# Kernel optimization log

Hardware: AMD Instinct MI355X
Metric: run time of the kernel (lower is better)

## Reference

```python
import jax, jax.numpy as jnp
import numpy as np

NC, M, D = 4, 512, 64
COMMITMENT_COST = 0.25


def setup_inputs() -> dict:
    key = jax.random.key(0)
    k1, k2 = jax.random.split(key)
    N = 65536
    x = jax.random.normal(k1, (N, NC * D), dtype=jnp.float32)
    # original init: uniform(-1/m, 1/m); randn*small keeps comparable scale
    embedding = jax.random.normal(k2, (NC, M, D), dtype=jnp.float32) * (1.0 / M)
    mask = jnp.ones((N, NC), dtype=jnp.float32)
    return {"x": x, "embedding": embedding, "mask": mask}


def reference(x, embedding, mask):
    nc, m, d = embedding.shape
    x_flat = x.reshape(-1, nc, d)                      # (N, nc, d)
    xd = jax.lax.stop_gradient(x_flat)                 # detached copy

    # squared-distance search expressed as a GEMM (same math as sum((x-e)^2)):
    x2 = jnp.sum(xd * xd, axis=-1)[:, :, None]
    e2 = jnp.sum(embedding * embedding, axis=-1)[None, :, :]
    xe = jnp.einsum('ncd,cmd->ncm', xd, embedding)
    distances = x2 - 2.0 * xe + e2

    indices = jnp.argmin(distances, axis=-1)           # (N, nc) int
    # gather nearest code vectors: (N, nc, d)
    quantized = embedding[jnp.arange(nc)[None, :], indices]
    quantized = quantized * mask[..., None]

    codebook_loss = jnp.mean((jax.lax.stop_gradient(x_flat) - quantized) ** 2)
    e_latent_loss = jnp.mean((x_flat - jax.lax.stop_gradient(quantized)) ** 2)
    commitment_loss = COMMITMENT_COST * e_latent_loss

    # straight-through estimator
    quantized_st = x_flat + jax.lax.stop_gradient(quantized - x_flat)
    quantized_st = quantized_st.reshape(x.shape)

    # perplexity via per-codebook histogram (avoids N x nc x m one-hot)
    counts = jax.vmap(lambda idx: jnp.bincount(idx, length=m))(indices.T)  # (nc, m)
    avg_probs = counts.astype(x.dtype) / x_flat.shape[0]
    perplexity = jnp.exp(-jnp.sum(avg_probs * jnp.log(avg_probs + 1e-10)))

    return (quantized_st, commitment_loss, codebook_loss, perplexity, indices)
```

## Files before the change

kernel.cpp:

```cpp
#include <hip/hip_runtime.h>
#include <math.h>
#include <float.h>

#define NTOK 65536
#define NCB  4
#define MCODE 512
#define DIM  64

#define QST_SIZE (NTOK * NCB * DIM)
#define IDX_OFF  (QST_SIZE + 3)

#define TOK_TILE  128

#define WS_EH 0
#define WS_EL 262144
#define WS_D0 524288
#define WS_CNT 532480
#define WS_LOSS 540672

typedef _Float16 half8 __attribute__((ext_vector_type(8)));
typedef float floatx16 __attribute__((ext_vector_type(16)));

__global__ __launch_bounds__(256) void prep_kernel(const float* __restrict__ emb,
                                                   _Float16* __restrict__ ehf,
                                                   _Float16* __restrict__ elf,
                                                   float* __restrict__ d0p,
                                                   int* __restrict__ counts,
                                                   float* __restrict__ lossSum) {
    int row = blockIdx.x * 256 + threadIdx.x;
    if (row >= NCB * MCODE) return;
    const int c   = row >> 9;
    const int n   = row & 511;
    const int nt  = n >> 5;
    const int r5  = n & 31;
    const float* src = emb + (size_t)row * DIM;

    float s = 0.f;
#pragma unroll
    for (int ch = 0; ch < 4; ++ch) {
#pragma unroll
        for (int h = 0; h < 2; ++h) {
            half8 hv, lv;
#pragma unroll
            for (int t = 0; t < 8; ++t) {
                float e = src[ch * 16 + h * 8 + t];
                s += e * e;
                float f = e * 512.0f;
                _Float16 hi = (_Float16)f;
                float r = f - (float)hi;
                hv[t] = hi;
                lv[t] = (_Float16)r;
            }
            size_t off = ((size_t)((c * 16 + nt) * 4 + ch)) * 512 + (h * 32 + r5) * 8;
            *(half8*)(ehf + off) = hv;
            *(half8*)(elf + off) = lv;
        }
    }
    d0p[row] = -256.0f * s;
    counts[row] = 0;
    if (row == 0) *lossSum = 0.f;
}

__global__ __launch_bounds__(256) void vq_main(const float* __restrict__ x,
                                               const float* __restrict__ emb,
                                               const float* __restrict__ mask,
                                               const _Float16* __restrict__ ehf,
                                               const _Float16* __restrict__ elf,
                                               const float* __restrict__ d0p,
                                               int* __restrict__ counts,
                                               float* __restrict__ lossSum,
                                               float* __restrict__ outQ,
                                               float* __restrict__ outIdx) {
    __shared__ int   Is[TOK_TILE];
    __shared__ float wls[4];

    const int tid  = threadIdx.x;
    const int c    = blockIdx.y;
    const int n0tk = blockIdx.x * TOK_TILE;
    const int lane = tid & 63;
    const int w    = tid >> 6;
    const int l31  = lane & 31;
    const int hi   = lane >> 5;
    const int hi4  = hi * 4;

    half8 Bh[4], Bl[4];
    {
        const float* xr = x + (size_t)(n0tk + w * 32 + l31) * (NCB * DIM) + c * DIM + hi * 8;
#pragma unroll
        for (int ch = 0; ch < 4; ++ch) {
            float fv[8];
            *(float4*)(fv)     = *(const float4*)(xr + ch * 16);
            *(float4*)(fv + 4) = *(const float4*)(xr + ch * 16 + 4);
            half8 h8, l8;
#pragma unroll
            for (int t = 0; t < 8; ++t) {
                float f = fv[t];
                _Float16 hh = (_Float16)f;
                h8[t] = hh;
                l8[t] = (_Float16)(f - (float)hh);
            }
            Bh[ch] = h8;
            Bl[ch] = l8;
        }
    }

    const _Float16* Ah_base = ehf + (size_t)c * (16 * 4 * 512) + (size_t)lane * 8;
    const _Float16* Al_base = elf + (size_t)c * (16 * 4 * 512) + (size_t)lane * 8;
    const float*    d0c     = d0p + c * MCODE;

    float maxv = -FLT_MAX;
    int   maxn = 0;

    for (int nt = 0; nt < 16; ++nt) {
        const _Float16* pah = Ah_base + (size_t)nt * 2048;
        const _Float16* pal = Al_base + (size_t)nt * 2048;
        half8 Ah0 = *(const half8*)(pah);
        half8 Ah1 = *(const half8*)(pah + 512);
        half8 Ah2 = *(const half8*)(pah + 1024);
        half8 Ah3 = *(const half8*)(pah + 1536);
        half8 Al0 = *(const half8*)(pal);
        half8 Al1 = *(const half8*)(pal + 512);
        half8 Al2 = *(const half8*)(pal + 1024);
        half8 Al3 = *(const half8*)(pal + 1536);

        const float* dpt = d0c + nt * 32 + hi4;
        float4 d40 = *(const float4*)(dpt);
        float4 d41 = *(const float4*)(dpt + 8);
        float4 d42 = *(const float4*)(dpt + 16);
        float4 d43 = *(const float4*)(dpt + 24);
        floatx16 acc;
        acc[0]  = d40.x; acc[1]  = d40.y; acc[2]  = d40.z; acc[3]  = d40.w;
        acc[4]  = d41.x; acc[5]  = d41.y; acc[6]  = d41.z; acc[7]  = d41.w;
        acc[8]  = d42.x; acc[9]  = d42.y; acc[10] = d42.z; acc[11] = d42.w;
        acc[12] = d43.x; acc[13] = d43.y; acc[14] = d43.z; acc[15] = d43.w;

        acc = __builtin_amdgcn_mfma_f32_32x32x16_f16(Ah0, Bh[0], acc, 0, 0, 0);
        acc = __builtin_amdgcn_mfma_f32_32x32x16_f16(Al0, Bh[0], acc, 0, 0, 0);
        acc = __builtin_amdgcn_mfma_f32_32x32x16_f16(Ah0, Bl[0], acc, 0, 0, 0);
        acc = __builtin_amdgcn_mfma_f32_32x32x16_f16(Ah1, Bh[1], acc, 0, 0, 0);
        acc = __builtin_amdgcn_mfma_f32_32x32x16_f16(Al1, Bh[1], acc, 0, 0, 0);
        acc = __builtin_amdgcn_mfma_f32_32x32x16_f16(Ah1, Bl[1], acc, 0, 0, 0);
        acc = __builtin_amdgcn_mfma_f32_32x32x16_f16(Ah2, Bh[2], acc, 0, 0, 0);
        acc = __builtin_amdgcn_mfma_f32_32x32x16_f16(Al2, Bh[2], acc, 0, 0, 0);
        acc = __builtin_amdgcn_mfma_f32_32x32x16_f16(Ah2, Bl[2], acc, 0, 0, 0);
        acc = __builtin_amdgcn_mfma_f32_32x32x16_f16(Ah3, Bh[3], acc, 0, 0, 0);
        acc = __builtin_amdgcn_mfma_f32_32x32x16_f16(Al3, Bh[3], acc, 0, 0, 0);
        acc = __builtin_amdgcn_mfma_f32_32x32x16_f16(Ah3, Bl[3], acc, 0, 0, 0);

        const int nbase = nt * 32 + hi4;
#pragma unroll
        for (int r = 0; r < 16; ++r) {
            float m = acc[r];
            int   n = nbase + ((r & 3) + 8 * (r >> 2));
            if (m > maxv) { maxv = m; maxn = n; }
        }
    }

    {
        float ov = __shfl_xor(maxv, 32);
        int   on = __shfl_xor(maxn, 32);
        if (ov > maxv || (ov == maxv && on < maxn)) { maxv = ov; maxn = on; }
    }

    if (hi == 0) {
        Is[w * 32 + l31] = maxn;
        atomicAdd(&counts[c * MCODE + maxn], 1);
        outIdx[(size_t)(n0tk + w * 32 + l31) * NCB + c] = (float)maxn;
    }
    __syncthreads();

    float lloss = 0.f;
#pragma unroll
    for (int i = 0; i < 8; ++i) {
        int q = tid + i * 256;
        int tok = q >> 4, d4 = q & 15;
        int idx = Is[tok];
        float mv = mask[(size_t)(n0tk + tok) * NCB + c];
        float4 e4 = *(const float4*)(emb + ((size_t)c * MCODE + idx) * DIM + d4 * 4);
        float4 x4 = *(const float4*)(x + (size_t)(n0tk + tok) * (NCB * DIM) + c * DIM + d4 * 4);
        float qx = e4.x * mv, qy = e4.y * mv, qz = e4.z * mv, qw = e4.w * mv;
        float4 o;
        o.x = x4.x + (qx - x4.x);
        o.y = x4.y + (qy - x4.y);
        o.z = x4.z + (qz - x4.z);
        o.w = x4.w + (qw - x4.w);
        *(float4*)(outQ + (size_t)(n0tk + tok) * (NCB * DIM) + c * DIM + d4 * 4) = o;
        float dx = x4.x - qx, dy = x4.y - qy, dz = x4.z - qz, dw = x4.w - qw;
        lloss += dx * dx + dy * dy + dz * dz + dw * dw;
    }
#pragma unroll
    for (int off = 32; off > 0; off >>= 1) lloss += __shfl_xor(lloss, off);
    if ((tid & 63) == 0) wls[tid >> 6] = lloss;
    __syncthreads();
    if (tid == 0) {
        float s = wls[0] + wls[1] + wls[2] + wls[3];
        atomicAdd(lossSum, s);
    }
}

__global__ __launch_bounds__(256) void finalize_kernel(const int* __restrict__ counts,
                                                       const float* __restrict__ lossSum,
                                                       float* __restrict__ out) {
    __shared__ float wls[4];
    int tid = threadIdx.x;
    float s = 0.f;
#pragma unroll
    for (int i = 0; i < 8; ++i) {
        int j = tid + i * 256;
        float p = (float)counts[j] * (1.0f / 65536.0f);
        s += p * logf(p + 1e-10f);
    }
#pragma unroll
    for (int off = 32; off > 0; off >>= 1) s += __shfl_xor(s, off);
    if ((tid & 63) == 0) wls[tid >> 6] = s;
    __syncthreads();
    if (tid == 0) {
        float tot = wls[0] + wls[1] + wls[2] + wls[3];
        float L = *lossSum * (1.0f / (float)QST_SIZE);
        out[QST_SIZE + 0] = 0.25f * L;
        out[QST_SIZE + 1] = L;
        out[QST_SIZE + 2] = expf(-tot);
    }
}

extern "C" void kernel_launch(void* const* d_in, const int* in_sizes, int n_in,
                              void* d_out, int out_size, void* d_ws, size_t ws_size,
                              hipStream_t stream) {
    const float* x    = (const float*)d_in[0];
    const float* emb  = (const float*)d_in[1];
    const float* mask = (const float*)d_in[2];
    float* out = (float*)d_out;

    _Float16* ehf  = (_Float16*)((char*)d_ws + WS_EH);
    _Float16* elf  = (_Float16*)((char*)d_ws + WS_EL);
    float* d0p     = (float*)((char*)d_ws + WS_D0);
    int*   counts  = (int*)((char*)d_ws + WS_CNT);
    float* lossSum = (float*)((char*)d_ws + WS_LOSS);

    prep_kernel<<<dim3(8), dim3(256), 0, stream>>>(emb, ehf, elf, d0p, counts, lossSum);
    vq_main<<<dim3(NTOK / TOK_TILE, NCB), dim3(256), 0, stream>>>(
        x, emb, mask, ehf, elf, d0p, counts, lossSum, out, out + IDX_OFF);
    finalize_kernel<<<dim3(1), dim3(256), 0, stream>>>(counts, lossSum, out);
}
```

Baseline: 211.3 us.

## Stage codebook tiles through double-buffered LDS with prefetch

Each block now loads the per-codebook fp16 hi/lo embedding tiles and the distance bias cooperatively into shared memory. The next tile is prefetched from global memory while the current one runs through MFMA, replacing the per-wave direct global loads in which every wave read the same codebook data. This cuts redundant global/L2 traffic and hides load latency, at the cost of a block-wide barrier per iteration and extra LDS use that may lower occupancy.

Result: faster. 202.6 us (-4.1%).

```diff
diff --git a/kernel.cpp b/kernel.cpp
--- a/kernel.cpp
+++ b/kernel.cpp
@@ -71,6 +71,8 @@
                                                float* __restrict__ lossSum,
                                                float* __restrict__ outQ,
                                                float* __restrict__ outIdx) {
+    __shared__ __align__(16) _Float16 As[2][4096];
+    __shared__ __align__(16) float d0s[MCODE];
     __shared__ int   Is[TOK_TILE];
     __shared__ float wls[4];
 
@@ -83,6 +85,14 @@
     const int hi   = lane >> 5;
     const int hi4  = hi * 4;
 
+    const _Float16* gEh = ehf + (size_t)c * (16 * 4 * 512);
+    const _Float16* gEl = elf + (size_t)c * (16 * 4 * 512);
+
+    float4 sh = *(const float4*)(gEh + tid * 8);
+    float4 sl = *(const float4*)(gEl + tid * 8);
+    float4 dstage;
+    if (tid < 128) dstage = *(const float4*)(d0p + c * MCODE + tid * 4);
+
     half8 Bh[4], Bl[4];
     {
         const float* xr = x + (size_t)(n0tk + w * 32 + l31) * (NCB * DIM) + c * DIM + hi * 8;
@@ -104,26 +114,35 @@
         }
     }
 
-    const _Float16* Ah_base = ehf + (size_t)c * (16 * 4 * 512) + (size_t)lane * 8;
-    const _Float16* Al_base = elf + (size_t)c * (16 * 4 * 512) + (size_t)lane * 8;
-    const float*    d0c     = d0p + c * MCODE;
+    *(float4*)((char*)&As[0][0]    + tid * 16) = sh;
+    *(float4*)((char*)&As[0][2048] + tid * 16) = sl;
+    if (tid < 128) *(float4*)(&d0s[tid * 4]) = dstage;
+    __syncthreads();
 
     float maxv = -FLT_MAX;
     int   maxn = 0;
 
     for (int nt = 0; nt < 16; ++nt) {
-        const _Float16* pah = Ah_base + (size_t)nt * 2048;
-        const _Float16* pal = Al_base + (size_t)nt * 2048;
-        half8 Ah0 = *(const half8*)(pah);
-        half8 Ah1 = *(const half8*)(pah + 512);
-        half8 Ah2 = *(const half8*)(pah + 1024);
-        half8 Ah3 = *(const half8*)(pah + 1536);
-        half8 Al0 = *(const half8*)(pal);
-        half8 Al1 = *(const half8*)(pal + 512);
-        half8 Al2 = *(const half8*)(pal + 1024);
-        half8 Al3 = *(const half8*)(pal + 1536);
-
-        const float* dpt = d0c + nt * 32 + hi4;
+        const int p = nt & 1;
+
+        float4 nh, nl;
+        if (nt < 15) {
+            nh = *(const float4*)(gEh + (nt + 1) * 2048 + tid * 8);
+            nl = *(const float4*)(gEl + (nt + 1) * 2048 + tid * 8);
+        }
+
+        const _Float16* ah = &As[p][0] + lane * 8;
+        const _Float16* al = &As[p][2048] + lane * 8;
+        half8 Ah0 = *(const half8*)(ah);
+        half8 Ah1 = *(const half8*)(ah + 512);
+        half8 Ah2 = *(const half8*)(ah + 1024);
+        half8 Ah3 = *(const half8*)(ah + 1536);
+        half8 Al0 = *(const half8*)(al);
+        half8 Al1 = *(const half8*)(al + 512);
+        half8 Al2 = *(const half8*)(al + 1024);
+        half8 Al3 = *(const half8*)(al + 1536);
+
+        const float* dpt = &d0s[nt * 32 + hi4];
         float4 d40 = *(const float4*)(dpt);
         float4 d41 = *(const float4*)(dpt + 8);
         float4 d42 = *(const float4*)(dpt + 16);
@@ -154,6 +173,12 @@
             int   n = nbase + ((r & 3) + 8 * (r >> 2));
             if (m > maxv) { maxv = m; maxn = n; }
         }
+
+        if (nt < 15) {
+            *(float4*)((char*)&As[p ^ 1][0]    + tid * 16) = nh;
+            *(float4*)((char*)&As[p ^ 1][2048] + tid * 16) = nl;
+        }
+        __syncthreads();
     }
 
     {
```
